# Performance work log

Measured on AMD Instinct MI355X. Metric: run time of the kernel, lower is better.

The kernel has to match this reference:

```python
import jax, jax.numpy as jnp
import numpy as np

DIM = 512      # model dim
HEADS = 8
DH = DIM // HEADS          # 64, dim_head
M = DIM // 2               # 256, num_landmarks
ITERS = 6                  # pinv_iterations
K = 33                     # residual_conv_kernel (lucidrains default)
B, N = 4, 4096             # N divisible by M -> no padding branch


def setup_inputs() -> dict:
    key = jax.random.key(0)
    ks = jax.random.split(key, 5)
    s = 0.02
    return {
        "x": jax.random.normal(ks[0], (B, N, DIM), jnp.float32),
        "ln_w": jnp.ones((DIM,), jnp.float32),
        "ln_b": jnp.zeros((DIM,), jnp.float32),
        "w_qkv": jax.random.normal(ks[1], (DIM, 3 * HEADS * DH), jnp.float32) * s,
        "w_out": jax.random.normal(ks[2], (HEADS * DH, DIM), jnp.float32) * s,
        "b_out": jnp.zeros((DIM,), jnp.float32),
        "w_conv": jax.random.normal(ks[3], (HEADS, 1, K, 1), jnp.float32) * s,  # depthwise Conv2d (h,1,33,1)
    }


def _moore_penrose_pinv(x, iters=ITERS):
    # Newton-Schulz iterative pseudo-inverse, as in lucidrains nystrom-attention
    abs_x = jnp.abs(x)
    col = abs_x.sum(-1)
    row = abs_x.sum(-2)
    z = jnp.swapaxes(x, -1, -2) / (jnp.max(col) * jnp.max(row))  # global max, matching torch.max
    I = jnp.eye(x.shape[-1], dtype=x.dtype)
    for _ in range(iters):
        xz = x @ z
        z = 0.25 * z @ (13.0 * I - xz @ (15.0 * I - xz @ (7.0 * I - xz)))
    return z


def reference(x, ln_w, ln_b, w_qkv, w_out, b_out, w_conv):
    b, n, d = x.shape
    # LayerNorm (biased variance, eps=1e-5 as torch default)
    mu = jnp.mean(x, -1, keepdims=True)
    var = jnp.mean(jnp.square(x - mu), -1, keepdims=True)
    xn = (x - mu) / jnp.sqrt(var + 1e-5) * ln_w + ln_b

    qkv = xn @ w_qkv                                   # [b,n,3*h*dh]
    q, k, v = jnp.split(qkv, 3, axis=-1)
    split = lambda t: t.reshape(b, n, HEADS, DH).transpose(0, 2, 1, 3)  # [b,h,n,dh]
    q, k, v = split(q), split(k), split(v)
    q = q * (DH ** -0.5)

    l = n // M                                         # tokens per landmark
    q_l = q.reshape(b, HEADS, M, l, DH).mean(axis=3)   # [b,h,m,dh]
    k_l = k.reshape(b, HEADS, M, l, DH).mean(axis=3)

    sim1 = jnp.einsum('bhid,bhjd->bhij', q, k_l)       # [b,h,n,m]
    sim2 = jnp.einsum('bhid,bhjd->bhij', q_l, k_l)     # [b,h,m,m]
    sim3 = jnp.einsum('bhid,bhjd->bhij', q_l, k)       # [b,h,m,n]
    a1 = jax.nn.softmax(sim1, -1)
    a2 = jax.nn.softmax(sim2, -1)
    a3 = jax.nn.softmax(sim3, -1)

    a2_inv = _moore_penrose_pinv(a2)
    out = (a1 @ a2_inv) @ (a3 @ v)                     # [b,h,n,dh]

    # depthwise residual conv over sequence dim (kernel (33,1), groups=heads)
    res = jax.lax.conv_general_dilated(
        v, w_conv, window_strides=(1, 1),
        padding=((K // 2, K // 2), (0, 0)),
        dimension_numbers=('NCHW', 'OIHW', 'NCHW'),
        feature_group_count=HEADS)
    out = out + res

    out = out.transpose(0, 2, 1, 3).reshape(b, n, HEADS * DH)
    out = out @ w_out + b_out
    return x + out
```

## Files before the change

kernel.cpp:

```cpp
#include <hip/hip_runtime.h>
#include <cstdint>

typedef __bf16 bf16;
typedef __bf16 bf16x8 __attribute__((ext_vector_type(8)));
typedef float  f32x4  __attribute__((ext_vector_type(4)));

__device__ __forceinline__ void glds16(const void* g, void* l) {
  __builtin_amdgcn_global_load_lds((const __attribute__((address_space(1))) void*)g,
                                   (__attribute__((address_space(3))) void*)l, 16, 0, 0);
}

__global__ __launch_bounds__(256) void prep_w(const float* __restrict__ wqkv, const float* __restrict__ wout,
                                              bf16* __restrict__ wqkvT, bf16* __restrict__ woutT) {
  int idx = blockIdx.x * 256 + threadIdx.x;
  if (idx < 98304) {
    int r8 = idx & 63, c = idx >> 6;
    bf16 o[8];
#pragma unroll
    for (int e = 0; e < 8; e++) o[e] = (bf16)wqkv[(long)(r8 * 8 + e) * 1536 + c];
    *(uint4*)(wqkvT + (long)c * 512 + r8 * 8) = *(uint4*)o;
  } else {
    int j = idx - 98304;
    int r8 = j & 63, c = j >> 6;
    bf16 o[8];
#pragma unroll
    for (int e = 0; e < 8; e++) o[e] = (bf16)wout[(long)(r8 * 8 + e) * 512 + c];
    *(uint4*)(woutT + (long)c * 512 + r8 * 8) = *(uint4*)o;
  }
}

__global__ __launch_bounds__(64) void ln_kernel(const float* __restrict__ x,
    const float* __restrict__ w, const float* __restrict__ b, bf16* __restrict__ xn) {
  long row = blockIdx.x;
  int t = threadIdx.x;
  const float* rp = x + row * 512 + t * 8;
  float4 p0 = *(const float4*)rp;
  float4 p1 = *(const float4*)(rp + 4);
  float vals[8] = {p0.x, p0.y, p0.z, p0.w, p1.x, p1.y, p1.z, p1.w};
  float s = 0.f, s2 = 0.f;
#pragma unroll
  for (int e = 0; e < 8; e++) { s += vals[e]; s2 += vals[e] * vals[e]; }
#pragma unroll
  for (int o = 32; o > 0; o >>= 1) { s += __shfl_xor(s, o); s2 += __shfl_xor(s2, o); }
  float mu = s * (1.f / 512.f);
  float var = s2 * (1.f / 512.f) - mu * mu;
  float rstd = rsqrtf(var + 1e-5f);
  float4 w0 = *(const float4*)(w + t * 8), w1 = *(const float4*)(w + t * 8 + 4);
  float4 b0 = *(const float4*)(b + t * 8), b1 = *(const float4*)(b + t * 8 + 4);
  float wv[8] = {w0.x, w0.y, w0.z, w0.w, w1.x, w1.y, w1.z, w1.w};
  float bv[8] = {b0.x, b0.y, b0.z, b0.w, b1.x, b1.y, b1.z, b1.w};
  bf16 outv[8];
#pragma unroll
  for (int e = 0; e < 8; e++) outv[e] = (bf16)((vals[e] - mu) * rstd * wv[e] + bv[e]);
  *(uint4*)(xn + row * 512 + t * 8) = *(uint4*)outv;
}

enum { MODE_BF16 = 1, MODE_QKV = 2, MODE_RESID = 3, MODE_XZ = 4, MODE_DIAG = 5, MODE_Y0 = 6, MODE_ZY = 7 };

template <int BM, int MODE>
__global__ __launch_bounds__(256) void gemm_g(
    const bf16* __restrict__ A, const bf16* __restrict__ B, void* __restrict__ C,
    int N, int K, long sA, long sB, long sC, float alpha, float cdiag,
    const float* __restrict__ resid, const float* __restrict__ bias,
    bf16* __restrict__ aux0, bf16* __restrict__ aux1, bf16* __restrict__ aux2) {
  constexpr int BK = 32, BN = BM;
  __shared__ __align__(16) bf16 As[BM * BK];
  __shared__ __align__(16) bf16 Bs[BN * BK];
  const int tid = threadIdx.x, lane = tid & 63, wave = tid >> 6;
  const int quad = lane >> 4, l16 = lane & 15;
  constexpr int WN = (BN >= 128) ? 2 : 1;
  constexpr int WM = 4 / WN;
  constexpr int TM = BM / (WM * 16), TN = BN / (WN * 16);
  constexpr int ISS = BM / 64;
  const int wm0 = (wave / WN) * (BM / WM);
  const int wn0 = (wave % WN) * (BN / WN);
  const int bm0 = blockIdx.x * BM, bn0 = blockIdx.y * BN;
  const bf16* Ab = A + (long)blockIdx.z * sA;
  const bf16* Bb = B + (long)(MODE == MODE_ZY ? (blockIdx.z & 31) : blockIdx.z) * sB;
  const int srow = lane >> 2, scol = (lane & 3) * 8;

  f32x4 zero = {0.f, 0.f, 0.f, 0.f};
  f32x4 acc[TM][TN];
#pragma unroll
  for (int i = 0; i < TM; i++)
#pragma unroll
    for (int j = 0; j < TN; j++) acc[i][j] = zero;

  for (int k0 = 0; k0 < K; k0 += BK) {
#pragma unroll
    for (int t = 0; t < ISS; t++) {
      int seg = wave * ISS + t;
      glds16(&Ab[(long)(bm0 + seg * 16 + srow) * K + k0 + scol], &As[seg * 512]);
      glds16(&Bb[(long)(bn0 + seg * 16 + srow) * K + k0 + scol], &Bs[seg * 512]);
    }
    __syncthreads();
    bf16x8 af[TM], bfr[TN];
#pragma unroll
    for (int i = 0; i < TM; i++)
      af[i] = *(const bf16x8*)&As[(wm0 + i * 16 + l16) * BK + quad * 8];
#pragma unroll
    for (int j = 0; j < TN; j++)
      bfr[j] = *(const bf16x8*)&Bs[(wn0 + j * 16 + l16) * BK + quad * 8];
#pragma unroll
    for (int i = 0; i < TM; i++)
#pragma unroll
      for (int j = 0; j < TN; j++)
        acc[i][j] = __builtin_amdgcn_mfma_f32_16x16x32_bf16(af[i], bfr[j], acc[i][j], 0, 0, 0);
    __syncthreads();
  }

  const long cb = (long)blockIdx.z * sC;
  float rscale = 1.f;
  if (MODE == MODE_Y0) rscale = 1.f / (resid[0] * resid[1]);
#pragma unroll
  for (int i = 0; i < TM; i++)
#pragma unroll
    for (int j = 0; j < TN; j++)
#pragma unroll
      for (int r = 0; r < 4; r++) {
        int row = bm0 + wm0 + i * 16 + quad * 4 + r;
        int col = bn0 + wn0 + j * 16 + l16;
        float v = acc[i][j][r] * alpha;
        if (MODE == MODE_BF16) {
          ((bf16*)C)[cb + (long)row * N + col] = (bf16)v;
        } else if (MODE == MODE_QKV) {
          int b = row >> 12, n = row & 4095;
          int which = col >> 9, h = (col >> 6) & 7, d = col & 63;
          long o = ((long)(b * 8 + h) * 4096 + n) * 64 + d;
          if (which == 0) aux0[o] = (bf16)(v * 0.125f);
          else if (which == 1) aux1[o] = (bf16)v;
          else aux2[o] = (bf16)v;
        } else if (MODE == MODE_Y0) {
          long o = cb + (long)row * N + col;
          float vv = v * rscale;
          aux0[o] = (bf16)vv;
          aux1[o] = (bf16)(((row == col) ? cdiag : 0.f) - vv);
        } else if (MODE == MODE_ZY) {
          long o = cb + (long)row * N + col;
          ((bf16*)C)[o] = (bf16)v;
          if (blockIdx.z >= 32) aux1[o - 2097152] = (bf16)(((row == col) ? cdiag : 0.f) - v);
        } else if (MODE == MODE_DIAG) {
          ((bf16*)C)[cb + (long)row * N + col] = (bf16)(((row == col) ? cdiag : 0.f) - v);
        } else {
          long o = (long)row * N + col;
          ((float*)C)[o] = v + bias[col] + resid[o];
        }
      }
}

template <int BM, int BN, bool BT, int MODE>
__global__ __launch_bounds__(256) void gemm_k(
    const bf16* __restrict__ A, const bf16* __restrict__ B, void* __restrict__ C,
    int M, int N, int K, long sA, long sB, long sC, float alpha, float cdiag,
    const float* __restrict__ resid, const float* __restrict__ bias,
    bf16* __restrict__ aux0, bf16* __restrict__ aux1, bf16* __restrict__ aux2) {
  constexpr int BK = 32, LDST = 40;
  __shared__ __align__(16) bf16 As[BM * LDST];
  __shared__ __align__(16) bf16 Bs[BN * LDST];
  const int tid = threadIdx.x, lane = tid & 63, wave = tid >> 6;
  const int quad = lane >> 4, l16 = lane & 15;
  constexpr int WN = (BN >= 128) ? 2 : 1;
  constexpr int WM = 4 / WN;
  constexpr int TM = BM / (WM * 16), TN = BN / (WN * 16);
  const int wm0 = (wave / WN) * (BM / WM);
  const int wn0 = (wave % WN) * (BN / WN);
  const int bm0 = blockIdx.x * BM, bn0 = blockIdx.y * BN;
  const bf16* Ab = A + (long)blockIdx.z * sA;
  const bf16* Bb = B + (long)blockIdx.z * sB;

  f32x4 zero = {0.f, 0.f, 0.f, 0.f};
  f32x4 acc[TM][TN];
#pragma unroll
  for (int i = 0; i < TM; i++)
#pragma unroll
    for (int j = 0; j < TN; j++) acc[i][j] = zero;

  for (int k0 = 0; k0 < K; k0 += BK) {
    for (int c = tid; c < BM * 4; c += 256) {
      int r = c >> 2, cv = (c & 3) * 8;
      *(uint4*)&As[r * LDST + cv] = *(const uint4*)&Ab[(long)(bm0 + r) * K + k0 + cv];
    }
    if (BT) {
      for (int c = tid; c < BN * 4; c += 256) {
        int r = c >> 2, cv = (c & 3) * 8;
        *(uint4*)&Bs[r * LDST + cv] = *(const uint4*)&Bb[(long)(bn0 + r) * K + k0 + cv];
      }
    } else {
      for (int c = tid; c < BN * 4; c += 256) {
        int kk = c / (BN / 8), nv = (c % (BN / 8)) * 8;
        uint4 tmp = *(const uint4*)&Bb[(long)(k0 + kk) * N + bn0 + nv];
        const bf16* tv = (const bf16*)&tmp;
#pragma unroll
        for (int e = 0; e < 8; e++) Bs[(nv + e) * LDST + kk] = tv[e];
      }
    }
    __syncthreads();
    bf16x8 af[TM], bfr[TN];
#pragma unroll
    for (int i = 0; i < TM; i++)
      af[i] = *(const bf16x8*)&As[(wm0 + i * 16 + l16) * LDST + quad * 8];
#pragma unroll
    for (int j = 0; j < TN; j++)
      bfr[j] = *(const bf16x8*)&Bs[(wn0 + j * 16 + l16) * LDST + quad * 8];
#pragma unroll
    for (int i = 0; i < TM; i++)
#pragma unroll
      for (int j = 0; j < TN; j++)
        acc[i][j] = __builtin_amdgcn_mfma_f32_16x16x32_bf16(af[i], bfr[j], acc[i][j], 0, 0, 0);
    __syncthreads();
  }

  const long cb = (long)blockIdx.z * sC;
#pragma unroll
  for (int i = 0; i < TM; i++)
#pragma unroll
    for (int j = 0; j < TN; j++)
#pragma unroll
      for (int r = 0; r < 4; r++) {
        int row = bm0 + wm0 + i * 16 + quad * 4 + r;
        int col = bn0 + wn0 + j * 16 + l16;
        float v = acc[i][j][r] * alpha;
        if (MODE == MODE_BF16) {
          ((bf16*)C)[cb + (long)row * N + col] = (bf16)v;
        } else if (MODE == MODE_DIAG) {
          ((bf16*)C)[cb + (long)row * N + col] = (bf16)(((row == col) ? cdiag : 0.f) - v);
        } else {
          long o = (long)row * N + col;
          ((float*)C)[o] = v + bias[col] + resid[o];
        }
      }
}

__global__ __launch_bounds__(256) void lm_kernel(const bf16* __restrict__ q, const bf16* __restrict__ k,
                                                 bf16* __restrict__ ql, bf16* __restrict__ kl) {
  int bh = blockIdx.x, mi = blockIdx.y * 4 + (threadIdx.x >> 6), d = threadIdx.x & 63;
  long base = ((long)bh * 4096 + mi * 16) * 64 + d;
  float sq = 0.f, sk = 0.f;
#pragma unroll
  for (int j = 0; j < 16; j++) { sq += (float)q[base + j * 64]; sk += (float)k[base + j * 64]; }
  long o = ((long)bh * 256 + mi) * 64 + d;
  ql[o] = (bf16)(sq * (1.f / 16.f));
  kl[o] = (bf16)(sk * (1.f / 16.f));
}

__global__ __launch_bounds__(256) void softmax256(bf16* __restrict__ buf) {
  long row = blockIdx.x;
  int t = threadIdx.x, lane = t & 63, wave = t >> 6;
  __shared__ float sm[4];
  float v = (float)buf[row * 256 + t];
  float m = v;
#pragma unroll
  for (int o = 32; o > 0; o >>= 1) m = fmaxf(m, __shfl_xor(m, o));
  if (lane == 0) sm[wave] = m;
  __syncthreads();
  m = fmaxf(fmaxf(sm[0], sm[1]), fmaxf(sm[2], sm[3]));
  float e = __expf(v - m);
  __syncthreads();
  float s = e;
#pragma unroll
  for (int o = 32; o > 0; o >>= 1) s += __shfl_xor(s, o);
  if (lane == 0) sm[wave] = s;
  __syncthreads();
  s = sm[0] + sm[1] + sm[2] + sm[3];
  buf[row * 256 + t] = (bf16)(e / s);
}

__global__ void init_scal(float* scal) { scal[0] = 1.0f; ((int*)scal)[1] = 0; }

__global__ __launch_bounds__(64) void red_col(const bf16* __restrict__ a2h, float* scal) {
  int bh = blockIdx.x;
  int j = blockIdx.y * 64 + threadIdx.x;
  float s = 0.f;
  const bf16* p = a2h + (long)bh * 65536 + j;
  for (int i = 0; i < 256; i++) s += (float)p[i * 256];
  atomicMax((int*)scal + 1, __float_as_int(s));
}

__global__ __launch_bounds__(256) void z0_k(const bf16* __restrict__ a2h,
                                            const float* __restrict__ scal, bf16* __restrict__ z) {
  int bh = blockIdx.x, i = blockIdx.y, j = threadIdx.x;
  float inv = 1.f / (scal[0] * scal[1]);
  float v = (float)a2h[((long)bh * 256 + i) * 256 + j];
  z[((long)bh * 256 + j) * 256 + i] = (bf16)(v * inv);
}

__global__ __launch_bounds__(256) void wt_k(const bf16* __restrict__ W, bf16* __restrict__ WT) {
  int bh = blockIdx.x, tid = threadIdx.x;
  const bf16* wb = W + (long)bh * 16384;
  bf16* wtb = WT + (long)bh * 16384;
  for (int i = tid; i < 2048; i += 256) {
    int n = i >> 3, d8 = (i & 7) * 8;
    uint4 pk = *(const uint4*)&wb[n * 64 + d8];
    const bf16* pv = (const bf16*)&pk;
#pragma unroll
    for (int e = 0; e < 8; e++) wtb[(d8 + e) * 256 + n] = pv[e];
  }
}

__global__ __launch_bounds__(256) void f3_partial(const bf16* __restrict__ ql,
    const bf16* __restrict__ k, const bf16* __restrict__ v,
    float* __restrict__ Opart, float* __restrict__ lpart) {
  const int mt = blockIdx.x, ns = blockIdx.y, bh = blockIdx.z;
  const int tid = threadIdx.x, lane = tid & 63, wave = tid >> 6;
  const int quad = lane >> 4, l16 = lane & 15;
  const int wr0 = mt * 128 + wave * 32;
  __shared__ __align__(16) bf16 vT[64][72];
  __shared__ __align__(16) bf16 Pts[4][32][72];

  const bf16* qlb = ql + (long)bh * 16384;
  const bf16* kb  = k + (long)bh * 262144;
  const bf16* vb  = v + (long)bh * 262144;

  bf16x8 aq[2][2];
#pragma unroll
  for (int ti = 0; ti < 2; ti++)
#pragma unroll
    for (int ki = 0; ki < 2; ki++)
      aq[ti][ki] = *(const bf16x8*)&qlb[(wr0 + ti * 16 + l16) * 64 + ki * 32 + quad * 8];

  f32x4 zero = {0.f, 0.f, 0.f, 0.f};
  f32x4 Oacc[2][4];
#pragma unroll
  for (int i = 0; i < 2; i++)
#pragma unroll
    for (int j = 0; j < 4; j++) Oacc[i][j] = zero;
  float lacc[2][4] = {};

  for (int c = 0; c < 8; c++) {
    int n0c = ns * 512 + c * 64;
    __syncthreads();
    for (int i = tid; i < 512; i += 256) {
      int nn = i >> 3, d8 = (i & 7) * 8;
      uint4 pk = *(const uint4*)&vb[(long)(n0c + nn) * 64 + d8];
      const bf16* pv = (const bf16*)&pk;
#pragma unroll
      for (int e = 0; e < 8; e++) vT[d8 + e][nn] = pv[e];
    }
    __syncthreads();

    f32x4 sacc[2][4];
#pragma unroll
    for (int i = 0; i < 2; i++)
#pragma unroll
      for (int j = 0; j < 4; j++) sacc[i][j] = zero;
#pragma unroll
    for (int ki = 0; ki < 2; ki++) {
      bf16x8 bk[4];
#pragma unroll
      for (int tj = 0; tj < 4; tj++)
        bk[tj] = *(const bf16x8*)&kb[(long)(n0c + tj * 16 + l16) * 64 + ki * 32 + quad * 8];
#pragma unroll
      for (int ti = 0; ti < 2; ti++)
#pragma unroll
        for (int tj = 0; tj < 4; tj++)
          sacc[ti][tj] = __builtin_amdgcn_mfma_f32_16x16x32_bf16(aq[ti][ki], bk[tj], sacc[ti][tj], 0, 0, 0);
    }
#pragma unroll
    for (int ti = 0; ti < 2; ti++)
#pragma unroll
      for (int tj = 0; tj < 4; tj++)
#pragma unroll
        for (int r = 0; r < 4; r++) {
          float e = __expf(sacc[ti][tj][r]);
          lacc[ti][r] += e;
          Pts[wave][ti * 16 + quad * 4 + r][tj * 16 + l16] = (bf16)e;
        }
#pragma unroll
    for (int ki = 0; ki < 2; ki++) {
      bf16x8 ap[2], bv[4];
#pragma unroll
      for (int ti = 0; ti < 2; ti++)
        ap[ti] = *(const bf16x8*)&Pts[wave][ti * 16 + l16][ki * 32 + quad * 8];
#pragma unroll
      for (int tj = 0; tj < 4; tj++)
        bv[tj] = *(const bf16x8*)&vT[tj * 16 + l16][ki * 32 + quad * 8];
#pragma unroll
      for (int ti = 0; ti < 2; ti++)
#pragma unroll
        for (int tj = 0; tj < 4; tj++)
          Oacc[ti][tj] = __builtin_amdgcn_mfma_f32_16x16x32_bf16(ap[ti], bv[tj], Oacc[ti][tj], 0, 0, 0);
    }
  }

#pragma unroll
  for (int ti = 0; ti < 2; ti++)
#pragma unroll
    for (int r = 0; r < 4; r++) {
#pragma unroll
      for (int o = 1; o < 16; o <<= 1) lacc[ti][r] += __shfl_xor(lacc[ti][r], o);
    }
  long pb = ((long)bh * 8 + ns) * 256;
#pragma unroll
  for (int ti = 0; ti < 2; ti++)
#pragma unroll
    for (int r = 0; r < 4; r++) {
      int row = wr0 + ti * 16 + quad * 4 + r;
      if (l16 == 0) lpart[pb + row] = lacc[ti][r];
#pragma unroll
      for (int tj = 0; tj < 4; tj++)
        Opart[(pb + row) * 64 + tj * 16 + l16] = Oacc[ti][tj][r];
    }
}

__global__ __launch_bounds__(256) void f3_combine(const float* __restrict__ Opart,
    const float* __restrict__ lpart, bf16* __restrict__ a3v) {
  int row = blockIdx.x * 4 + (threadIdx.x >> 6);
  int d = threadIdx.x & 63;
  int bh = row >> 8, m = row & 255;
  float so = 0.f, sl = 0.f;
#pragma unroll
  for (int s = 0; s < 8; s++) {
    long pb = ((long)bh * 8 + s) * 256 + m;
    so += Opart[pb * 64 + d];
    sl += lpart[pb];
  }
  a3v[(long)row * 64 + d] = (bf16)(so / sl);
}

__global__ __launch_bounds__(256) void f1_attn(const bf16* __restrict__ q,
    const bf16* __restrict__ kl, const bf16* __restrict__ WT, const bf16* __restrict__ v,
    const float* __restrict__ wconv, bf16* __restrict__ xattn) {
  const int nt = blockIdx.x, bh = blockIdx.y;
  const int h = bh & 7, b = bh >> 3, n0 = nt * 64;
  const int tid = threadIdx.x, lane = tid & 63, wave = tid >> 6;
  const int quad = lane >> 4, l16 = lane & 15;
  __shared__ __align__(16) bf16 PtsBuf[64 * 264];
  __shared__ float red[4][64];
  __shared__ float linv[64];
  bf16 (*Pts)[264] = (bf16(*)[264])PtsBuf;
  bf16 (*vsT)[104] = (bf16(*)[104])PtsBuf;

  const bf16* qb  = q + (long)bh * 262144;
  const bf16* klb = kl + (long)bh * 16384;
  const bf16* wtb = WT + (long)bh * 16384;
  const bf16* vb  = v + (long)bh * 262144;

  float wreg = (lane < 33) ? wconv[h * 33 + lane] : 0.f;

  f32x4 zero = {0.f, 0.f, 0.f, 0.f};
  f32x4 sacc[4][4];
#pragma unroll
  for (int i = 0; i < 4; i++)
#pragma unroll
    for (int j = 0; j < 4; j++) sacc[i][j] = zero;
#pragma unroll
  for (int ki = 0; ki < 2; ki++) {
    bf16x8 aq[4], bk[4];
#pragma unroll
    for (int ti = 0; ti < 4; ti++)
      aq[ti] = *(const bf16x8*)&qb[(long)(n0 + ti * 16 + l16) * 64 + ki * 32 + quad * 8];
#pragma unroll
    for (int tj = 0; tj < 4; tj++)
      bk[tj] = *(const bf16x8*)&klb[(long)(wave * 64 + tj * 16 + l16) * 64 + ki * 32 + quad * 8];
#pragma unroll
    for (int ti = 0; ti < 4; ti++)
#pragma unroll
      for (int tj = 0; tj < 4; tj++)
        sacc[ti][tj] = __builtin_amdgcn_mfma_f32_16x16x32_bf16(aq[ti], bk[tj], sacc[ti][tj], 0, 0, 0);
  }
  float ps[4][4] = {};
#pragma unroll
  for (int ti = 0; ti < 4; ti++)
#pragma unroll
    for (int tj = 0; tj < 4; tj++)
#pragma unroll
      for (int r = 0; r < 4; r++) {
        float e = __expf(sacc[ti][tj][r]);
        ps[ti][r] += e;
        Pts[ti * 16 + quad * 4 + r][wave * 64 + tj * 16 + l16] = (bf16)e;
      }
#pragma unroll
  for (int ti = 0; ti < 4; ti++)
#pragma unroll
    for (int r = 0; r < 4; r++) {
#pragma unroll
      for (int o = 1; o < 16; o <<= 1) ps[ti][r] += __shfl_xor(ps[ti][r], o);
      if (l16 == 0) red[wave][ti * 16 + quad * 4 + r] = ps[ti][r];
    }
  __syncthreads();
  if (tid < 64) linv[tid] = 1.f / (red[0][tid] + red[1][tid] + red[2][tid] + red[3][tid]);
  __syncthreads();

  const int r0 = wave * 16;
  f32x4 Oacc[4];
#pragma unroll
  for (int j = 0; j < 4; j++) Oacc[j] = zero;
#pragma unroll
  for (int ki = 0; ki < 8; ki++) {
    bf16x8 ap = *(const bf16x8*)&Pts[r0 + l16][ki * 32 + quad * 8];
    bf16x8 bw[4];
#pragma unroll
    for (int tj = 0; tj < 4; tj++)
      bw[tj] = *(const bf16x8*)&wtb[(long)(tj * 16 + l16) * 256 + ki * 32 + quad * 8];
#pragma unroll
    for (int tj = 0; tj < 4; tj++)
      Oacc[tj] = __builtin_amdgcn_mfma_f32_16x16x32_bf16(ap, bw[tj], Oacc[tj], 0, 0, 0);
  }
  __syncthreads();

  for (int i = tid; i < 768; i += 256) {
    int r = i >> 3, d8 = (i & 7) * 8;
    int n = n0 - 16 + r;
    uint4 val = {0u, 0u, 0u, 0u};
    if (n >= 0 && n < 4096) val = *(const uint4*)&vb[(long)n * 64 + d8];
    const bf16* pv = (const bf16*)&val;
#pragma unroll
    for (int e = 0; e < 8; e++) vsT[d8 + e][r] = pv[e];
  }
  __syncthreads();

  f32x4 Cacc[4];
#pragma unroll
  for (int j = 0; j < 4; j++) Cacc[j] = zero;
#pragma unroll
  for (int ki = 0; ki < 3; ki++) {
    if (ki * 32 + 31 < r0 || ki * 32 > r0 + 47) continue;
    bf16x8 av;
#pragma unroll
    for (int j = 0; j < 8; j++) {
      int idx = ki * 32 + quad * 8 + j - r0 - l16;
      float wv = __shfl(wreg, idx & 63);
      av[j] = (idx >= 0 && idx < 33) ? (bf16)wv : (bf16)0.f;
    }
    bf16x8 bv[4];
#pragma unroll
    for (int tj = 0; tj < 4; tj++)
      bv[tj] = *(const bf16x8*)&vsT[tj * 16 + l16][ki * 32 + quad * 8];
#pragma unroll
    for (int tj = 0; tj < 4; tj++)
      Cacc[tj] = __builtin_amdgcn_mfma_f32_16x16x32_bf16(av, bv[tj], Cacc[tj], 0, 0, 0);
  }

#pragma unroll
  for (int rr = 0; rr < 4; rr++) {
    int row = r0 + quad * 4 + rr;
    float inv = linv[row];
    int n = n0 + row;
#pragma unroll
    for (int tj = 0; tj < 4; tj++) {
      int d = tj * 16 + l16;
      xattn[(((long)b * 4096 + n) << 9) + (h << 6) + d] = (bf16)(Oacc[tj][rr] * inv + Cacc[tj][rr]);
    }
  }
}

extern "C" void kernel_launch(void* const* d_in, const int* in_sizes, int n_in,
                              void* d_out, int out_size, void* d_ws, size_t ws_size,
                              hipStream_t stream) {
  (void)in_sizes; (void)n_in; (void)out_size; (void)ws_size;
  const float* x      = (const float*)d_in[0];
  const float* ln_w   = (const float*)d_in[1];
  const float* ln_b   = (const float*)d_in[2];
  const float* w_qkv  = (const float*)d_in[3];
  const float* w_out  = (const float*)d_in[4];
  const float* b_out  = (const float*)d_in[5];
  const float* w_conv = (const float*)d_in[6];
  float* out = (float*)d_out;

  char* ws = (char*)d_ws;
  const size_t MB = 1u << 20;
  bf16* q      = (bf16*)(ws + 0 * MB);
  bf16* k      = (bf16*)(ws + 16 * MB);
  bf16* v      = (bf16*)(ws + 32 * MB);
  bf16* xn     = (bf16*)(ws + 48 * MB);
  bf16* a2_h   = (bf16*)(ws + 48 * MB);
  bf16* pbuf   = (bf16*)(ws + 52 * MB);
  bf16* qbuf   = (bf16*)(ws + 56 * MB);
  bf16* rbuf   = (bf16*)(ws + 60 * MB);
  bf16* bufA   = (bf16*)(ws + 64 * MB);
  bf16* bufB   = (bf16*)(ws + 72 * MB);
  float* Opart = (float*)(ws + 48 * MB);
  float* lpart = (float*)(ws + 72 * MB);
  bf16* xattn  = (bf16*)(ws + 73 * MB);
  bf16* wqkvT  = (bf16*)(ws + 73 * MB);
  bf16* ql     = (bf16*)(ws + 89 * MB);
  bf16* kl     = (bf16*)(ws + 90 * MB);
  bf16* a3v    = (bf16*)(ws + 91 * MB);
  bf16* W      = (bf16*)(ws + 92 * MB);
  bf16* WT     = (bf16*)(ws + 93 * MB);
  bf16* woutT  = (bf16*)(ws + 94 * MB);
  float* scal  = (float*)(ws + 94 * MB + 512 * 1024);

  prep_w<<<512, 256, 0, stream>>>(w_qkv, w_out, wqkvT, woutT);
  ln_kernel<<<16384, 64, 0, stream>>>(x, ln_w, ln_b, xn);

  gemm_g<128, MODE_QKV><<<dim3(128, 12, 1), 256, 0, stream>>>(
      xn, wqkvT, nullptr, 1536, 512, 0, 0, 0, 1.f, 0.f, nullptr, nullptr, q, k, v);

  lm_kernel<<<dim3(32, 64), 256, 0, stream>>>(q, k, ql, kl);

  gemm_g<64, MODE_BF16><<<dim3(4, 4, 32), 256, 0, stream>>>(
      ql, kl, a2_h, 256, 64, 16384, 16384, 65536, 1.f, 0.f, nullptr, nullptr, nullptr, nullptr, nullptr);
  softmax256<<<8192, 256, 0, stream>>>(a2_h);

  init_scal<<<1, 1, 0, stream>>>(scal);
  red_col<<<dim3(32, 4), 64, 0, stream>>>(a2_h, scal);
  z0_k<<<dim3(32, 256), 256, 0, stream>>>(a2_h, scal, bufA);
  gemm_g<64, MODE_Y0><<<dim3(4, 4, 32), 256, 0, stream>>>(
      a2_h, a2_h, nullptr, 256, 256, 65536, 65536, 65536, 1.f, 7.f, scal, nullptr,
      bufA + 2097152, pbuf, nullptr);

  bf16* cur = bufA;
  bf16* nxt = bufB;
  for (int it = 0; it < 6; it++) {
    gemm_g<64, MODE_DIAG><<<dim3(4, 4, 32), 256, 0, stream>>>(
        cur + 2097152, pbuf, qbuf, 256, 256, 65536, 65536, 65536, 1.f, 15.f,
        nullptr, nullptr, nullptr, nullptr, nullptr);
    gemm_g<64, MODE_DIAG><<<dim3(4, 4, 32), 256, 0, stream>>>(
        cur + 2097152, qbuf, rbuf, 256, 256, 65536, 65536, 65536, 1.f, 13.f,
        nullptr, nullptr, nullptr, nullptr, nullptr);
    if (it < 5) {
      gemm_g<64, MODE_ZY><<<dim3(4, 4, 64), 256, 0, stream>>>(
          cur, rbuf, nxt, 256, 256, 65536, 65536, 65536, 0.25f, 7.f,
          nullptr, nullptr, nullptr, pbuf, nullptr);
    } else {
      gemm_g<64, MODE_BF16><<<dim3(4, 4, 32), 256, 0, stream>>>(
          cur, rbuf, nxt, 256, 256, 65536, 65536, 65536, 0.25f, 0.f,
          nullptr, nullptr, nullptr, nullptr, nullptr);
    }
    bf16* tmp = cur; cur = nxt; nxt = tmp;
  }

  f3_partial<<<dim3(2, 8, 32), 256, 0, stream>>>(ql, k, v, Opart, lpart);
  f3_combine<<<2048, 256, 0, stream>>>(Opart, lpart, a3v);

  gemm_k<64, 64, false, MODE_BF16><<<dim3(4, 1, 32), 256, 0, stream>>>(
      cur, a3v, W, 256, 64, 256, 65536, 16384, 16384, 1.f, 0.f, nullptr, nullptr, nullptr, nullptr, nullptr);
  wt_k<<<32, 256, 0, stream>>>(W, WT);

  f1_attn<<<dim3(64, 32), 256, 0, stream>>>(q, kl, WT, v, w_conv, xattn);

  gemm_g<128, MODE_RESID><<<dim3(128, 4, 1), 256, 0, stream>>>(
      xattn, woutT, out, 512, 512, 0, 0, 0, 1.f, 0.f, x, b_out, nullptr, nullptr, nullptr);
}
```

Before: 480.8 us.

## Load full-K tiles once with XOR swizzle for small pinv GEMMs; prefetch V in f1_attn

Adds a specialized gemm_ns kernel for the 256x256 (and K=64) batched Newton-Schulz GEMMs. It loads the whole K extent of A and B tiles into LDS in one shot with an XOR-swizzled layout, so the per-BK-step sync loop and its LDS bank conflicts go away. It also issues the V-halo global loads in f1_attn early into registers so they overlap the attention compute. The cost is more LDS per block (64 KB at K=256), which lowers occupancy, and extra registers in f1_attn.

```diff
diff --git a/kernel.cpp b/kernel.cpp
--- a/kernel.cpp
+++ b/kernel.cpp
@@ -56,6 +56,80 @@
 }
 
 enum { MODE_BF16 = 1, MODE_QKV = 2, MODE_RESID = 3, MODE_XZ = 4, MODE_DIAG = 5, MODE_Y0 = 6, MODE_ZY = 7 };
+
+template <int KDIM, int MODE>
+__global__ __launch_bounds__(256) void gemm_ns(
+    const bf16* __restrict__ A, const bf16* __restrict__ B, void* __restrict__ C,
+    int N, long sA, long sB, long sC, float alpha, float cdiag,
+    const float* __restrict__ scal, bf16* __restrict__ aux0, bf16* __restrict__ aux1) {
+  constexpr int BM = 64;
+  __shared__ __align__(16) bf16 As[BM * KDIM];
+  __shared__ __align__(16) bf16 Bs[BM * KDIM];
+  const int tid = threadIdx.x, lane = tid & 63, wave = tid >> 6;
+  const int quad = lane >> 4, l16 = lane & 15;
+  constexpr int LPR = KDIM / 8;
+  constexpr int CPW = (BM * KDIM / 512) / 4;
+  constexpr int RPC = 64 / LPR;
+  const int bm0 = blockIdx.x * BM, bn0 = blockIdx.y * BM;
+  const bf16* Ab = A + (long)blockIdx.z * sA;
+  const bf16* Bb = B + (long)(MODE == MODE_ZY ? (blockIdx.z & 31) : blockIdx.z) * sB;
+
+  const int rin = lane / LPR, gr = lane % LPR;
+#pragma unroll
+  for (int t = 0; t < CPW; t++) {
+    int seg = wave * CPW + t;
+    int row = seg * RPC + rin;
+    int scol = 8 * (gr ^ (row & 7));
+    glds16(&Ab[(long)(bm0 + row) * KDIM + scol], &As[seg * 512]);
+    glds16(&Bb[(long)(bn0 + row) * KDIM + scol], &Bs[seg * 512]);
+  }
+  __syncthreads();
+
+  f32x4 zero = {0.f, 0.f, 0.f, 0.f};
+  f32x4 acc[4];
+#pragma unroll
+  for (int j = 0; j < 4; j++) acc[j] = zero;
+  const int arow = wave * 16 + l16;
+  const int aswz = (l16 & 7) * 8;
+#pragma unroll
+  for (int ki = 0; ki < KDIM / 32; ki++) {
+    int cph = (ki * 32 + quad * 8) ^ aswz;
+    bf16x8 af = *(const bf16x8*)&As[arow * KDIM + cph];
+    bf16x8 bfr[4];
+#pragma unroll
+    for (int j = 0; j < 4; j++)
+      bfr[j] = *(const bf16x8*)&Bs[(j * 16 + l16) * KDIM + cph];
+#pragma unroll
+    for (int j = 0; j < 4; j++)
+      acc[j] = __builtin_amdgcn_mfma_f32_16x16x32_bf16(af, bfr[j], acc[j], 0, 0, 0);
+  }
+
+  const long cb = (long)blockIdx.z * sC;
+  float rscale = 1.f;
+  if (MODE == MODE_Y0) rscale = 1.f / (scal[0] * scal[1]);
+#pragma unroll
+  for (int j = 0; j < 4; j++)
+#pragma unroll
+    for (int r = 0; r < 4; r++) {
+      int row = bm0 + wave * 16 + quad * 4 + r;
+      int col = bn0 + j * 16 + l16;
+      float v = acc[j][r] * alpha;
+      if (MODE == MODE_BF16) {
+        ((bf16*)C)[cb + (long)row * N + col] = (bf16)v;
+      } else if (MODE == MODE_Y0) {
+        long o = cb + (long)row * N + col;
+        float vv = v * rscale;
+        aux0[o] = (bf16)vv;
+        aux1[o] = (bf16)(((row == col) ? cdiag : 0.f) - vv);
+      } else if (MODE == MODE_ZY) {
+        long o = cb + (long)row * N + col;
+        ((bf16*)C)[o] = (bf16)v;
+        if (blockIdx.z >= 32) aux1[o - 2097152] = (bf16)(((row == col) ? cdiag : 0.f) - v);
+      } else if (MODE == MODE_DIAG) {
+        ((bf16*)C)[cb + (long)row * N + col] = (bf16)(((row == col) ? cdiag : 0.f) - v);
+      }
+    }
+}
 
 template <int BM, int MODE>
 __global__ __launch_bounds__(256) void gemm_g(
@@ -76,7 +150,7 @@
   const int wn0 = (wave % WN) * (BN / WN);
   const int bm0 = blockIdx.x * BM, bn0 = blockIdx.y * BN;
   const bf16* Ab = A + (long)blockIdx.z * sA;
-  const bf16* Bb = B + (long)(MODE == MODE_ZY ? (blockIdx.z & 31) : blockIdx.z) * sB;
+  const bf16* Bb = B + (long)blockIdx.z * sB;
   const int srow = lane >> 2, scol = (lane & 3) * 8;
 
   f32x4 zero = {0.f, 0.f, 0.f, 0.f};
@@ -110,8 +184,6 @@
   }
 
   const long cb = (long)blockIdx.z * sC;
-  float rscale = 1.f;
-  if (MODE == MODE_Y0) rscale = 1.f / (resid[0] * resid[1]);
 #pragma unroll
   for (int i = 0; i < TM; i++)
 #pragma unroll
@@ -121,26 +193,13 @@
         int row = bm0 + wm0 + i * 16 + quad * 4 + r;
         int col = bn0 + wn0 + j * 16 + l16;
         float v = acc[i][j][r] * alpha;
-        if (MODE == MODE_BF16) {
-          ((bf16*)C)[cb + (long)row * N + col] = (bf16)v;
-        } else if (MODE == MODE_QKV) {
+        if (MODE == MODE_QKV) {
           int b = row >> 12, n = row & 4095;
           int which = col >> 9, h = (col >> 6) & 7, d = col & 63;
           long o = ((long)(b * 8 + h) * 4096 + n) * 64 + d;
           if (which == 0) aux0[o] = (bf16)(v * 0.125f);
           else if (which == 1) aux1[o] = (bf16)v;
           else aux2[o] = (bf16)v;
-        } else if (MODE == MODE_Y0) {
-          long o = cb + (long)row * N + col;
-          float vv = v * rscale;
-          aux0[o] = (bf16)vv;
-          aux1[o] = (bf16)(((row == col) ? cdiag : 0.f) - vv);
-        } else if (MODE == MODE_ZY) {
-          long o = cb + (long)row * N + col;
-          ((bf16*)C)[o] = (bf16)v;
-          if (blockIdx.z >= 32) aux1[o - 2097152] = (bf16)(((row == col) ? cdiag : 0.f) - v);
-        } else if (MODE == MODE_DIAG) {
-          ((bf16*)C)[cb + (long)row * N + col] = (bf16)(((row == col) ? cdiag : 0.f) - v);
         } else {
           long o = (long)row * N + col;
           ((float*)C)[o] = v + bias[col] + resid[o];
@@ -222,11 +281,6 @@
         float v = acc[i][j][r] * alpha;
         if (MODE == MODE_BF16) {
           ((bf16*)C)[cb + (long)row * N + col] = (bf16)v;
-        } else if (MODE == MODE_DIAG) {
-          ((bf16*)C)[cb + (long)row * N + col] = (bf16)(((row == col) ? cdiag : 0.f) - v);
-        } else {
-          long o = (long)row * N + col;
-          ((float*)C)[o] = v + bias[col] + resid[o];
         }
       }
 }
@@ -437,6 +491,17 @@
 
   float wreg = (lane < 33) ? wconv[h * 33 + lane] : 0.f;
 
+  uint4 vstage[3];
+#pragma unroll
+  for (int t = 0; t < 3; t++) {
+    int i = tid + t * 256;
+    int r = i >> 3, d8 = (i & 7) * 8;
+    int n = n0 - 16 + r;
+    uint4 val = {0u, 0u, 0u, 0u};
+    if (n >= 0 && n < 4096) val = *(const uint4*)&vb[(long)n * 64 + d8];
+    vstage[t] = val;
+  }
+
   f32x4 zero = {0.f, 0.f, 0.f, 0.f};
   f32x4 sacc[4][4];
 #pragma unroll
@@ -498,12 +563,11 @@
   }
   __syncthreads();
 
-  for (int i = tid; i < 768; i += 256) {
+#pragma unroll
+  for (int t = 0; t < 3; t++) {
+    int i = tid + t * 256;
     int r = i >> 3, d8 = (i & 7) * 8;
-    int n = n0 - 16 + r;
-    uint4 val = {0u, 0u, 0u, 0u};
-    if (n >= 0 && n < 4096) val = *(const uint4*)&vb[(long)n * 64 + d8];
-    const bf16* pv = (const bf16*)&val;
+    const bf16* pv = (const bf16*)&vstage[t];
 #pragma unroll
     for (int e = 0; e < 8; e++) vsT[d8 + e][r] = pv[e];
   }
@@ -589,34 +653,34 @@
 
   lm_kernel<<<dim3(32, 64), 256, 0, stream>>>(q, k, ql, kl);
 
-  gemm_g<64, MODE_BF16><<<dim3(4, 4, 32), 256, 0, stream>>>(
-      ql, kl, a2_h, 256, 64, 16384, 16384, 65536, 1.f, 0.f, nullptr, nullptr, nullptr, nullptr, nullptr);
+  gemm_ns<64, MODE_BF16><<<dim3(4, 4, 32), 256, 0, stream>>>(
+      ql, kl, a2_h, 256, 16384, 16384, 65536, 1.f, 0.f, nullptr, nullptr, nullptr);
   softmax256<<<8192, 256, 0, stream>>>(a2_h);
 
   init_scal<<<1, 1, 0, stream>>>(scal);
   red_col<<<dim3(32, 4), 64, 0, stream>>>(a2_h, scal);
   z0_k<<<dim3(32, 256), 256, 0, stream>>>(a2_h, scal, bufA);
-  gemm_g<64, MODE_Y0><<<dim3(4, 4, 32), 256, 0, stream>>>(
-      a2_h, a2_h, nullptr, 256, 256, 65536, 65536, 65536, 1.f, 7.f, scal, nullptr,
-      bufA + 2097152, pbuf, nullptr);
+  gemm_ns<256, MODE_Y0><<<dim3(4, 4, 32), 256, 0, stream>>>(
+      a2_h, a2_h, nullptr, 256, 65536, 65536, 65536, 1.f, 7.f, scal,
+      bufA + 2097152, pbuf);
 
   bf16* cur = bufA;
   bf16* nxt = bufB;
   for (int it = 0; it < 6; it++) {
-    gemm_g<64, MODE_DIAG><<<dim3(4, 4, 32), 256, 0, stream>>>(
-        cur + 2097152, pbuf, qbuf, 256, 256, 65536, 65536, 65536, 1.f, 15.f,
-        nullptr, nullptr, nullptr, nullptr, nullptr);
-    gemm_g<64, MODE_DIAG><<<dim3(4, 4, 32), 256, 0, stream>>>(
-        cur + 2097152, qbuf, rbuf, 256, 256, 65536, 65536, 65536, 1.f, 13.f,
-        nullptr, nullptr, nullptr, nullptr, nullptr);
+    gemm_ns<256, MODE_DIAG><<<dim3(4, 4, 32), 256, 0, stream>>>(
+        cur + 2097152, pbuf, qbuf, 256, 65536, 65536, 65536, 1.f, 15.f,
+        nullptr, nullptr, nullptr);
+    gemm_ns<256, MODE_DIAG><<<dim3(4, 4, 32), 256, 0, stream>>>(
+        cur + 2097152, qbuf, rbuf, 256, 65536, 65536, 65536, 1.f, 13.f,
+        nullptr, nullptr, nullptr);
     if (it < 5) {
-      gemm_g<64, MODE_ZY><<<dim3(4, 4, 64), 256, 0, stream>>>(
-          cur, rbuf, nxt, 256, 256, 65536, 65536, 65536, 0.25f, 7.f,
-          nullptr, nullptr, nullptr, pbuf, nullptr);
+      gemm_ns<256, MODE_ZY><<<dim3(4, 4, 64), 256, 0, stream>>>(
+          cur, rbuf, nxt, 256, 65536, 65536, 65536, 0.25f, 7.f,
+          nullptr, nullptr, pbuf);
     } else {
-      gemm_g<64, MODE_BF16><<<dim3(4, 4, 32), 256, 0, stream>>>(
-          cur, rbuf, nxt, 256, 256, 65536, 65536, 65536, 0.25f, 0.f,
-          nullptr, nullptr, nullptr, nullptr, nullptr);
+      gemm_ns<256, MODE_BF16><<<dim3(4, 4, 32), 256, 0, stream>>>(
+          cur, rbuf, nxt, 256, 65536, 65536, 65536, 0.25f, 0.f,
+          nullptr, nullptr, nullptr);
     }
     bf16* tmp = cur; cur = nxt; nxt = tmp;
   }
```

After: 459.3 us. 1.05x faster.
